# Kernel optimization log

Measured on AMD Instinct MI355X. Metric: run time of the kernel, lower is better.

The kernel has to match this reference:

```python
import jax, jax.numpy as jnp
import numpy as np

# ---- static config (matches init_kwargs) ----
BATCH = 8; SEQ_LEN = 1024; ENC_IN = 7; PRED_LEN = 96
D_MODEL = 512; N_HEADS = 8; D_HEAD = D_MODEL // N_HEADS
D_FF = 2048; E_LAYERS = 2; FACTOR = 5
PATCH = 16; STRIDE = 8; PAD = 8
N_PATCH = (SEQ_LEN + PAD - PATCH) // STRIDE + 1  # 128
NF = D_MODEL * N_PATCH


def _sin_pe(n, d):
    # sinusoidal positional embedding (Informer/TSLib PositionalEmbedding)
    pos = np.arange(n, dtype=np.float32)[:, None]
    div = np.exp(np.arange(0, d, 2, dtype=np.float32) * (-np.log(10000.0) / d))
    pe = np.zeros((n, d), dtype=np.float32)
    pe[:, 0::2] = np.sin(pos * div)
    pe[:, 1::2] = np.cos(pos * div)
    return jnp.asarray(pe)


def _ln(x, g, b, eps=1e-5):
    m = x.mean(-1, keepdims=True)
    v = x.var(-1, keepdims=True)
    return (x - m) / jnp.sqrt(v + eps) * g + b


def _prob_attention(q, k, v, layer_idx):
    # Informer ProbAttention, mask_flag=False. q,k,v: [B,H,L,Dh]
    B, H, L, Dh = q.shape
    u = min(int(FACTOR * np.ceil(np.log(L))), L)  # sample_k == n_top here (L_Q == L_K)
    skey = jax.random.fold_in(jax.random.key(42), layer_idx)
    samp = jax.random.randint(skey, (L, u), 0, L)          # random keys per query
    k_s = k[:, :, samp, :]                                  # [B,H,L,u,Dh]
    qk_s = jnp.einsum('bhld,bhlsd->bhls', q, k_s)           # sampled scores
    M = qk_s.max(-1) - qk_s.mean(-1)                        # sparsity measure [B,H,L]
    top = jax.lax.top_k(M, u)[1]                            # active query idx [B,H,u]
    q_r = jnp.take_along_axis(q, top[..., None], axis=2)    # [B,H,u,Dh]
    scores = jnp.einsum('bhud,bhld->bhul', q_r, k) / jnp.sqrt(jnp.asarray(Dh, q.dtype))
    attn = jax.nn.softmax(scores, axis=-1)
    upd = jnp.einsum('bhul,bhld->bhud', attn, v)            # [B,H,u,Dh]
    ctx = jnp.broadcast_to(v.mean(axis=2, keepdims=True), (B, H, L, Dh))
    bi = jnp.arange(B)[:, None, None]
    hi = jnp.arange(H)[None, :, None]
    ctx = ctx.at[bi, hi, top].set(upd)                      # scatter updated queries
    return ctx


def reference(x_enc, x_mark_enc, x_dec, x_mark_dec, patch_W,
              Wq, bq, Wk, bk, Wv, bv, Wo, bo,
              c1W, c1b, c2W, c2b, ln1g, ln1b, ln2g, ln2b,
              encg, encb, headW, headb):
    B, L, C = x_enc.shape
    # Normalize('Stat'): per-series mean/std over time
    mean = x_enc.mean(axis=1, keepdims=True)
    std = jnp.sqrt(x_enc.var(axis=1, keepdims=True) + 1e-5)
    xn = (x_enc - mean) / std
    # PatchEmbedding: [B,C,L] -> replication-pad -> unfold -> linear + pos emb
    xc = jnp.pad(xn.transpose(0, 2, 1), ((0, 0), (0, 0), (0, PAD)), mode='edge')
    idx = np.arange(N_PATCH)[:, None] * STRIDE + np.arange(PATCH)
    tok = xc[:, :, idx].reshape(B * C, N_PATCH, PATCH) @ patch_W.T  # [BC,N,dm]
    tok = tok + _sin_pe(N_PATCH, D_MODEL)
    # Transformer encoder with ProbAttention
    for l in range(E_LAYERS):
        Beff, N, _ = tok.shape
        q = (tok @ Wq[l].T + bq[l]).reshape(Beff, N, N_HEADS, D_HEAD).transpose(0, 2, 1, 3)
        k = (tok @ Wk[l].T + bk[l]).reshape(Beff, N, N_HEADS, D_HEAD).transpose(0, 2, 1, 3)
        v = (tok @ Wv[l].T + bv[l]).reshape(Beff, N, N_HEADS, D_HEAD).transpose(0, 2, 1, 3)
        ctx = _prob_attention(q, k, v, l).transpose(0, 2, 1, 3).reshape(Beff, N, D_MODEL)
        x1 = _ln(tok + ctx @ Wo[l].T + bo[l], ln1g[l], ln1b[l])
        y = jax.nn.gelu(x1 @ c1W[l].T + c1b[l], approximate=False)  # conv1d k=1 == linear
        y = y @ c2W[l].T + c2b[l]
        tok = _ln(x1 + y, ln2g[l], ln2b[l])
    tok = _ln(tok, encg, encb)
    # FlattenHead: [B,C,N,dm] -> [B,C,dm,N] -> flatten -> linear -> [B,pred,C]
    feat = tok.reshape(B, C, N_PATCH, D_MODEL).transpose(0, 1, 3, 2).reshape(B, C, NF)
    dec = (feat @ headW.T + headb).transpose(0, 2, 1)
    return dec * std + mean  # de-normalize


def setup_inputs():
    key = jax.random.key(0)
    ks = iter(jax.random.split(key, 40))
    def rn(shape, s=0.02):
        return jax.random.normal(next(ks), shape, jnp.float32) * s
    return {
        'x_enc': jax.random.normal(next(ks), (BATCH, SEQ_LEN, ENC_IN), jnp.float32),
        'x_mark_enc': jax.random.normal(next(ks), (BATCH, SEQ_LEN, 4), jnp.float32),
        'x_dec': jax.random.normal(next(ks), (BATCH, 144, ENC_IN), jnp.float32),
        'x_mark_dec': jax.random.normal(next(ks), (BATCH, 144, 4), jnp.float32),
        'patch_W': rn((D_MODEL, PATCH)),
        'Wq': rn((E_LAYERS, D_MODEL, D_MODEL)), 'bq': jnp.zeros((E_LAYERS, D_MODEL)),
        'Wk': rn((E_LAYERS, D_MODEL, D_MODEL)), 'bk': jnp.zeros((E_LAYERS, D_MODEL)),
        'Wv': rn((E_LAYERS, D_MODEL, D_MODEL)), 'bv': jnp.zeros((E_LAYERS, D_MODEL)),
        'Wo': rn((E_LAYERS, D_MODEL, D_MODEL)), 'bo': jnp.zeros((E_LAYERS, D_MODEL)),
        'c1W': rn((E_LAYERS, D_FF, D_MODEL)), 'c1b': jnp.zeros((E_LAYERS, D_FF)),
        'c2W': rn((E_LAYERS, D_MODEL, D_FF)), 'c2b': jnp.zeros((E_LAYERS, D_MODEL)),
        'ln1g': jnp.ones((E_LAYERS, D_MODEL)), 'ln1b': jnp.zeros((E_LAYERS, D_MODEL)),
        'ln2g': jnp.ones((E_LAYERS, D_MODEL)), 'ln2b': jnp.zeros((E_LAYERS, D_MODEL)),
        'encg': jnp.ones((D_MODEL,)), 'encb': jnp.zeros((D_MODEL,)),
        'headW': rn((PRED_LEN, NF)), 'headb': jnp.zeros((PRED_LEN,)),
    }
```

## Files before the change

### kernel.cpp

```cpp
#include <hip/hip_runtime.h>
#include <math.h>
#include <stdint.h>

#define SEQ   1024
#define CIN   7
#define NB    8
#define BC    56
#define NP    128
#define DM    512
#define NH    8
#define DH    64
#define DFF   2048
#define U     25
#define NTOK  (BC*NP)
#define PE_COEF (-9.210340371976184f / 512.0f)
#define HKB   256
#define HNB   256

typedef __attribute__((ext_vector_type(8))) short short8;
typedef __attribute__((ext_vector_type(4))) float f32x4;

__device__ __forceinline__ short f2bf(float x) {
    union { float f; uint32_t u; } v; v.f = x;
    uint32_t r = v.u + 0x7FFFu + ((v.u >> 16) & 1u);
    return (short)(r >> 16);
}
__device__ __forceinline__ float bf2f(short x) {
    union { uint32_t u; float f; } v; v.u = ((uint32_t)(uint16_t)x) << 16;
    return v.f;
}

__device__ __forceinline__ void gl_lds16(const void* g, void* s) {
    __builtin_amdgcn_global_load_lds((const __attribute__((address_space(1))) void*)g,
                                     (__attribute__((address_space(3))) void*)s, 16, 0, 0);
}

__global__ void stats_kernel(const float* __restrict__ x, float* __restrict__ mean,
                             float* __restrict__ stdv) {
    int bc = blockIdx.x; int b = bc / CIN, c = bc % CIN;
    const float* base = x + (size_t)b * SEQ * CIN + c;
    float s = 0.f, ss = 0.f;
    for (int i = threadIdx.x; i < SEQ; i += 256) {
        float v = base[(size_t)i * CIN];
        s += v; ss += v * v;
    }
    __shared__ float rs[256], rss[256];
    rs[threadIdx.x] = s; rss[threadIdx.x] = ss; __syncthreads();
    for (int o = 128; o > 0; o >>= 1) {
        if (threadIdx.x < o) { rs[threadIdx.x] += rs[threadIdx.x + o]; rss[threadIdx.x] += rss[threadIdx.x + o]; }
        __syncthreads();
    }
    if (threadIdx.x == 0) {
        float m = rs[0] / SEQ;
        float v = rss[0] / SEQ - m * m;
        mean[bc] = m;
        stdv[bc] = sqrtf(v + 1e-5f);
    }
}

__device__ __forceinline__ void tf_round(uint32_t& x0, uint32_t& x1, uint32_t r) {
    x0 += x1; x1 = (x1 << r) | (x1 >> (32u - r)); x1 ^= x0;
}
__device__ void threefry2x32(uint32_t k0, uint32_t k1, uint32_t x0, uint32_t x1,
                             uint32_t& o0, uint32_t& o1) {
    uint32_t ks[3] = { k0, k1, k0 ^ k1 ^ 0x1BD11BDAu };
    x0 += ks[0]; x1 += ks[1];
    const uint32_t rotA[4] = {13u, 15u, 26u, 6u}, rotB[4] = {17u, 29u, 16u, 24u};
    #pragma unroll
    for (int i = 0; i < 5; i++) {
        const uint32_t* rr = (i & 1) ? rotB : rotA;
        tf_round(x0, x1, rr[0]); tf_round(x0, x1, rr[1]);
        tf_round(x0, x1, rr[2]); tf_round(x0, x1, rr[3]);
        x0 += ks[(i + 1) % 3];
        x1 += ks[(i + 2) % 3] + (uint32_t)(i + 1);
    }
    o0 = x0; o1 = x1;
}

__global__ void prep_weights(const float* __restrict__ Wq, const float* __restrict__ Wk,
                             const float* __restrict__ Wv, const float* __restrict__ bq,
                             const float* __restrict__ bk, const float* __restrict__ bv,
                             const float* __restrict__ Wo, const float* __restrict__ c1W,
                             const float* __restrict__ c2W,
                             short* __restrict__ wqkv, float* __restrict__ bqkv,
                             short* __restrict__ wo_b, short* __restrict__ c1w_b,
                             short* __restrict__ c2w_b, int* __restrict__ samp) {
    int blk = blockIdx.x, tid = threadIdx.x;
    if (blk < 1536) {
        int idx = blk * 256 + tid;
        int k4 = idx & 127;
        int n  = (idx >> 7) % 1536;
        int l  = idx / (1536 * 128);
        int sel3 = n >> 9;
        int nn = n & 511;
        const float* src = sel3 == 0 ? Wq : sel3 == 1 ? Wk : Wv;
        float4 v = *(const float4*)(src + ((size_t)l * DM + nn) * DM + k4 * 4);
        short4 o; o.x = f2bf(v.x); o.y = f2bf(v.y); o.z = f2bf(v.z); o.w = f2bf(v.w);
        *(short4*)(wqkv + ((size_t)l * 1536 + n) * DM + k4 * 4) = o;
        if (k4 == 0) {
            const float* bsrc = sel3 == 0 ? bq : sel3 == 1 ? bk : bv;
            bqkv[l * 1536 + n] = bsrc[l * DM + nn];
        }
    } else if (blk < 6144) {
        const float* in; short* out; int i;
        if (blk < 2048)      { in = Wo;  out = wo_b;  i = (blk - 1536) * 256 + tid; }
        else if (blk < 4096) { in = c1W; out = c1w_b; i = (blk - 2048) * 256 + tid; }
        else                 { in = c2W; out = c2w_b; i = (blk - 4096) * 256 + tid; }
        float4 v = ((const float4*)in)[i];
        short4 o; o.x = f2bf(v.x); o.y = f2bf(v.y); o.z = f2bf(v.z); o.w = f2bf(v.w);
        ((short4*)out)[i] = o;
    } else {
        int l = blk - 6144;
        uint32_t s0, s1; threefry2x32(0u, 42u, 0u, (uint32_t)l, s0, s1);
        uint32_t a0, a1, b0, b1;
        threefry2x32(s0, s1, 0u, 2u, a0, a1);
        threefry2x32(s0, s1, 1u, 3u, b0, b1);
        uint32_t k20 = a1, k21 = b1;
        for (int i = tid; i < 1600; i += 256) {
            uint32_t o0, o1;
            threefry2x32(k20, k21, (uint32_t)i, (uint32_t)(1600 + i), o0, o1);
            samp[l * 3200 + i]        = (int)(o0 & 127u);
            samp[l * 3200 + 1600 + i] = (int)(o1 & 127u);
        }
    }
}

__global__ void patch_embed(const float* __restrict__ x, const float* __restrict__ pw,
                            const float* __restrict__ mean, const float* __restrict__ stdv,
                            float* __restrict__ tok, short* __restrict__ tokb) {
    int p = blockIdx.x, bc = blockIdx.y;
    int b = bc / CIN, c = bc % CIN;
    __shared__ float xs[16];
    if (threadIdx.x < 16) {
        int i = p * 8 + threadIdx.x;
        if (i > SEQ - 1) i = SEQ - 1;
        xs[threadIdx.x] = (x[(size_t)b * SEQ * CIN + (size_t)i * CIN + c] - mean[bc]) / stdv[bc];
    }
    __syncthreads();
    for (int d = threadIdx.x; d < DM; d += blockDim.x) {
        float acc = 0.f;
        const float* wr = pw + d * 16;
        #pragma unroll
        for (int t = 0; t < 16; t++) acc += xs[t] * wr[t];
        int k2 = d & ~1;
        float ang = (float)p * __expf((float)k2 * PE_COEF);
        acc += (d & 1) ? __cosf(ang) : __sinf(ang);
        size_t idx = ((size_t)bc * NP + p) * DM + d;
        tok[idx] = acc;
        tokb[idx] = f2bf(acc);
    }
}

template<int ACT, int OBF>
__global__ __launch_bounds__(256) void gemm_mfma(const short* __restrict__ A,
                                                 const short* __restrict__ W,
                                                 const float* __restrict__ bias,
                                                 float* __restrict__ Cf,
                                                 short* __restrict__ Cb,
                                                 int M, int N, int K) {
    __shared__ short LDSU[2][16384];
    int tid = threadIdx.x;
    int w = tid >> 6, lane = tid & 63;
    int row0 = blockIdx.x * 128, col0 = blockIdx.y * 128;
    int wrow = (w >> 1) * 64, wcol = (w & 1) * 64;
    int nt = K >> 6;
    f32x4 acc[4][4] = {};

    auto stage = [&](int b, int kt) {
        #pragma unroll
        for (int i = 0; i < 4; i++) {
            int L = i * 4096 + w * 1024 + lane * 16;
            int row = L >> 7;
            int cb  = L & 127;
            int scb = cb ^ ((row & 7) << 4);
            gl_lds16(A + (size_t)(row0 + row) * K + kt + (scb >> 1),
                     (char*)&LDSU[b][0] + i * 4096 + w * 1024);
            gl_lds16(W + (size_t)(col0 + row) * K + kt + (scb >> 1),
                     (char*)&LDSU[b][8192] + i * 4096 + w * 1024);
        }
    };

    stage(0, 0);
    __syncthreads();
    int cur = 0;
    for (int t = 0; t < nt; t++) {
        if (t + 1 < nt) stage(cur ^ 1, (t + 1) * 64);
        const char* Ab = (const char*)&LDSU[cur][0];
        const char* Bb = (const char*)&LDSU[cur][8192];
        #pragma unroll
        for (int ks = 0; ks < 2; ks++) {
            int cb = ks * 64 + ((lane >> 4) << 4);
            short8 af[4], bfr[4];
            #pragma unroll
            for (int m = 0; m < 4; m++) {
                int r = wrow + m * 16 + (lane & 15);
                af[m] = *(const short8*)(Ab + r * 128 + (cb ^ ((r & 7) << 4)));
            }
            #pragma unroll
            for (int n = 0; n < 4; n++) {
                int r = wcol + n * 16 + (lane & 15);
                bfr[n] = *(const short8*)(Bb + r * 128 + (cb ^ ((r & 7) << 4)));
            }
            #pragma unroll
            for (int m = 0; m < 4; m++)
                #pragma unroll
                for (int n = 0; n < 4; n++)
                    acc[m][n] = __builtin_amdgcn_mfma_f32_16x16x32_bf16(af[m], bfr[n], acc[m][n], 0, 0, 0);
        }
        __syncthreads();
        cur ^= 1;
    }

    #pragma unroll
    for (int m = 0; m < 4; m++) {
        int rbase = row0 + wrow + m * 16 + ((lane >> 4) << 2);
        #pragma unroll
        for (int n = 0; n < 4; n++) {
            int col = col0 + wcol + n * 16 + (lane & 15);
            float bval = bias[col];
            #pragma unroll
            for (int j = 0; j < 4; j++) {
                float v = acc[m][n][j] + bval;
                if (ACT == 1) {
                    float u = 0.7978845608f * (v + 0.044715f * v * v * v);
                    float e = exp2f(2.8853900817779268f * u);
                    v = v - v / (e + 1.0f);
                }
                if (OBF) Cb[(size_t)(rbase + j) * N + col] = f2bf(v);
                else     Cf[(size_t)(rbase + j) * N + col] = v;
            }
        }
    }
}

__global__ __launch_bounds__(256) void gemm_mfma64(const short* __restrict__ A,
                                                   const short* __restrict__ W,
                                                   const float* __restrict__ bias,
                                                   const float* __restrict__ resid,
                                                   float* __restrict__ Cf,
                                                   int M, int N, int K) {
    __shared__ short LDSU[2][12288];
    int tid = threadIdx.x;
    int w = tid >> 6, lane = tid & 63;
    int row0 = blockIdx.x * 64, col0 = blockIdx.y * 128;
    int nt = K >> 6;
    f32x4 acc[4][2] = {};

    auto stage = [&](int b, int kt) {
        #pragma unroll
        for (int i = 0; i < 2; i++) {
            int L = (i * 4 + w) * 1024 + lane * 16;
            int row = L >> 7, cb = L & 127;
            int scb = cb ^ ((row & 7) << 4);
            gl_lds16(A + (size_t)(row0 + row) * K + kt + (scb >> 1),
                     (char*)&LDSU[b][0] + (i * 4 + w) * 1024);
        }
        #pragma unroll
        for (int i = 0; i < 4; i++) {
            int L = (i * 4 + w) * 1024 + lane * 16;
            int row = L >> 7, cb = L & 127;
            int scb = cb ^ ((row & 7) << 4);
            gl_lds16(W + (size_t)(col0 + row) * K + kt + (scb >> 1),
                     (char*)&LDSU[b][4096] + (i * 4 + w) * 1024);
        }
    };

    stage(0, 0);
    __syncthreads();
    int cur = 0;
    for (int t = 0; t < nt; t++) {
        if (t + 1 < nt) stage(cur ^ 1, (t + 1) * 64);
        const char* Ab = (const char*)&LDSU[cur][0];
        const char* Bb = (const char*)&LDSU[cur][4096];
        #pragma unroll
        for (int ks = 0; ks < 2; ks++) {
            int cb = ks * 64 + ((lane >> 4) << 4);
            short8 af[4], bfr[2];
            #pragma unroll
            for (int m = 0; m < 4; m++) {
                int r = m * 16 + (lane & 15);
                af[m] = *(const short8*)(Ab + r * 128 + (cb ^ ((r & 7) << 4)));
            }
            #pragma unroll
            for (int n = 0; n < 2; n++) {
                int r = w * 32 + n * 16 + (lane & 15);
                bfr[n] = *(const short8*)(Bb + r * 128 + (cb ^ ((r & 7) << 4)));
            }
            #pragma unroll
            for (int m = 0; m < 4; m++)
                #pragma unroll
                for (int n = 0; n < 2; n++)
                    acc[m][n] = __builtin_amdgcn_mfma_f32_16x16x32_bf16(af[m], bfr[n], acc[m][n], 0, 0, 0);
        }
        __syncthreads();
        cur ^= 1;
    }

    #pragma unroll
    for (int m = 0; m < 4; m++) {
        int rbase = row0 + m * 16 + ((lane >> 4) << 2);
        #pragma unroll
        for (int n = 0; n < 2; n++) {
            int col = col0 + w * 32 + n * 16 + (lane & 15);
            float bval = bias[col];
            #pragma unroll
            for (int j = 0; j < 4; j++) {
                float v = acc[m][n][j] + bval;
                v += resid[(size_t)(rbase + j) * N + col];
                Cf[(size_t)(rbase + j) * N + col] = v;
            }
        }
    }
}

__global__ __launch_bounds__(256, 2) void attn_fused(const short* __restrict__ qkvb,
                                                     const int* __restrict__ samp,
                                                     short* __restrict__ ctxb) {
    __shared__ float Sbuf[64 * 130];
    __shared__ short Vt[64 * 128];
    __shared__ short Kls[128 * 64];
    __shared__ float Mv[128];
    __shared__ int   topl[32];
    __shared__ float vmean[64];
    __shared__ float vpart[256];

    float* Stop = Sbuf;
    short* Pb   = (short*)(Sbuf + 32 * 130);

    int bh = blockIdx.x, bc = bh >> 3, h = bh & 7;
    int tid = threadIdx.x, w = tid >> 6, lane = tid & 63;
    const short* base = qkvb + (size_t)bc * NP * 1536 + h * DH;
    short* cbase = ctxb + (size_t)bc * NP * DM + h * DH;

    for (int e = tid; e < 1024; e += 256) {
        int row = e >> 3, c8 = e & 7;
        short8 kv = *(const short8*)(base + (size_t)row * 1536 + 512 + c8 * 8);
        *(short8*)((char*)Kls + row * 128 + ((c8 * 16) ^ ((row & 7) << 4))) = kv;
        short8 vv = *(const short8*)(base + (size_t)row * 1536 + 1024 + c8 * 8);
        #pragma unroll
        for (int j = 0; j < 8; j++) {
            int d = c8 * 8 + j;
            *(short*)((char*)Vt + d * 256 + ((2 * row) ^ ((d & 7) << 4))) = vv[j];
        }
    }
    __syncthreads();
    {
        int d = tid & 63, part = tid >> 6;
        float s = 0.f;
        #pragma unroll
        for (int i4 = 0; i4 < 4; i4++) {
            short8 v = *(const short8*)((char*)Vt + d * 256 + ((part * 64 + i4 * 16) ^ ((d & 7) << 4)));
            #pragma unroll
            for (int j = 0; j < 8; j++) s += bf2f(v[j]);
        }
        vpart[part * 64 + d] = s;
    }

    for (int half = 0; half < 2; half++) {
        int ar = half * 64 + 16 * w + (lane & 15);
        const short* qp = base + (size_t)ar * 1536;
        short8 a0 = *(const short8*)(qp + (lane >> 4) * 8);
        short8 a1 = *(const short8*)(qp + 32 + (lane >> 4) * 8);
        #pragma unroll 2
        for (int ct = 0; ct < 8; ct++) {
            int br = ct * 16 + (lane & 15);
            int cb0 = (lane >> 4) * 16;
            short8 b0 = *(const short8*)((char*)Kls + br * 128 + (cb0 ^ ((br & 7) << 4)));
            short8 b1 = *(const short8*)((char*)Kls + br * 128 + ((cb0 + 64) ^ ((br & 7) << 4)));
            f32x4 acc = {};
            acc = __builtin_amdgcn_mfma_f32_16x16x32_bf16(a0, b0, acc, 0, 0, 0);
            acc = __builtin_amdgcn_mfma_f32_16x16x32_bf16(a1, b1, acc, 0, 0, 0);
            int r0 = 16 * w + ((lane >> 4) << 2);
            int c = ct * 16 + (lane & 15);
            #pragma unroll
            for (int j = 0; j < 4; j++) Sbuf[(r0 + j) * 130 + c] = acc[j] * 0.125f;
        }
        __syncthreads();
        if (tid < 64) {
            int r = half * 64 + tid;
            const int* sp = samp + r * U;
            const float* Srow = &Sbuf[tid * 130];
            float mx = -1e30f, sm = 0.f;
            #pragma unroll
            for (int s = 0; s < U; s++) { float v = Srow[sp[s]]; mx = fmaxf(mx, v); sm += v; }
            Mv[r] = mx - sm * (1.0f / U);
        } else if (half == 0 && tid < 128) {
            int d = tid - 64;
            vmean[d] = (vpart[d] + vpart[64 + d] + vpart[128 + d] + vpart[192 + d]) * (1.0f / 128.0f);
        }
        __syncthreads();
    }

    if (w == 0) {
        float v0 = Mv[lane], v1 = Mv[lane + 64];
        for (int it = 0; it < U; it++) {
            float bv; int bi;
            if (v1 > v0) { bv = v1; bi = lane + 64; } else { bv = v0; bi = lane; }
            #pragma unroll
            for (int o = 32; o > 0; o >>= 1) {
                float ov = __shfl_xor(bv, o);
                int   oi = __shfl_xor(bi, o);
                if (ov > bv || (ov == bv && oi < bi)) { bv = ov; bi = oi; }
            }
            if (lane == 0) topl[it] = bi;
            if (bi == lane) v0 = -1e30f;
            if (bi == lane + 64) v1 = -1e30f;
        }
    } else {
        for (int e = tid - 64; e < 128 * 16; e += 192) {
            int n = e >> 4, c4 = e & 15;
            short4 o;
            o.x = f2bf(vmean[c4 * 4 + 0]); o.y = f2bf(vmean[c4 * 4 + 1]);
            o.z = f2bf(vmean[c4 * 4 + 2]); o.w = f2bf(vmean[c4 * 4 + 3]);
            *(short4*)(cbase + (size_t)n * DM + c4 * 4) = o;
        }
    }
    __syncthreads();

    {
        int rt = w & 1, cth = w >> 1;
        int u = rt * 16 + (lane & 15);
        int qrow = topl[u < U ? u : U - 1];
        const short* qp = base + (size_t)qrow * 1536;
        short8 a0 = *(const short8*)(qp + (lane >> 4) * 8);
        short8 a1 = *(const short8*)(qp + 32 + (lane >> 4) * 8);
        #pragma unroll
        for (int cti = 0; cti < 4; cti++) {
            int ct = cth * 4 + cti;
            int br = ct * 16 + (lane & 15);
            int cb0 = (lane >> 4) * 16;
            short8 b0 = *(const short8*)((char*)Kls + br * 128 + (cb0 ^ ((br & 7) << 4)));
            short8 b1 = *(const short8*)((char*)Kls + br * 128 + ((cb0 + 64) ^ ((br & 7) << 4)));
            f32x4 acc = {};
            acc = __builtin_amdgcn_mfma_f32_16x16x32_bf16(a0, b0, acc, 0, 0, 0);
            acc = __builtin_amdgcn_mfma_f32_16x16x32_bf16(a1, b1, acc, 0, 0, 0);
            int r0 = rt * 16 + ((lane >> 4) << 2);
            int c = ct * 16 + (lane & 15);
            #pragma unroll
            for (int j = 0; j < 4; j++) Stop[(r0 + j) * 130 + c] = acc[j] * 0.125f;
        }
    }
    __syncthreads();

    for (int e = tid; e < 7 * 128; e += 256)
        Pb[(25 + (e >> 7)) * 128 + (e & 127)] = 0;
    for (int it = w; it < U; it += 4) {
        float s0 = Stop[it * 130 + lane], s1 = Stop[it * 130 + 64 + lane];
        float mx = fmaxf(s0, s1);
        #pragma unroll
        for (int o = 32; o > 0; o >>= 1) mx = fmaxf(mx, __shfl_xor(mx, o));
        float e0 = expf(s0 - mx), e1 = expf(s1 - mx);
        float sum = e0 + e1;
        #pragma unroll
        for (int o = 32; o > 0; o >>= 1) sum += __shfl_xor(sum, o);
        float inv = 1.0f / sum;
        int sw = (it & 7) << 4;
        *(short*)((char*)Pb + it * 256 + ((2 * lane) ^ sw))        = f2bf(e0 * inv);
        *(short*)((char*)Pb + it * 256 + ((2 * (64 + lane)) ^ sw)) = f2bf(e1 * inv);
    }
    __syncthreads();

    #pragma unroll
    for (int t = w * 2; t < w * 2 + 2; t++) {
        int rt = t >> 2, ct = t & 3;
        int pr = rt * 16 + (lane & 15);
        int vr = ct * 16 + (lane & 15);
        f32x4 acc = {};
        #pragma unroll
        for (int ks = 0; ks < 4; ks++) {
            int off = ks * 64 + (lane >> 4) * 16;
            short8 a = *(const short8*)((char*)Pb + pr * 256 + (off ^ ((pr & 7) << 4)));
            short8 b = *(const short8*)((char*)Vt + vr * 256 + (off ^ ((vr & 7) << 4)));
            acc = __builtin_amdgcn_mfma_f32_16x16x32_bf16(a, b, acc, 0, 0, 0);
        }
        int u0 = rt * 16 + ((lane >> 4) << 2), d = ct * 16 + (lane & 15);
        #pragma unroll
        for (int j = 0; j < 4; j++) {
            int u = u0 + j;
            if (u < U) cbase[(size_t)topl[u] * DM + d] = f2bf(acc[j]);
        }
    }
}

__global__ __launch_bounds__(256) void residual_ln(const float* __restrict__ a,
                                                   const float* __restrict__ g,
                                                   const float* __restrict__ beta,
                                                   float* __restrict__ out,
                                                   short* __restrict__ outb) {
    int row = blockIdx.x;
    int tid = threadIdx.x;
    const float* ar = a + (size_t)row * DM;
    float x0 = ar[tid], x1 = ar[tid + 256];
    __shared__ float rs[256], rss[256];
    rs[tid] = x0 + x1; rss[tid] = x0 * x0 + x1 * x1; __syncthreads();
    for (int o = 128; o > 0; o >>= 1) {
        if (tid < o) { rs[tid] += rs[tid + o]; rss[tid] += rss[tid + o]; }
        __syncthreads();
    }
    float m = rs[0] / DM;
    float var = rss[0] / DM - m * m;
    float r = rsqrtf(var + 1e-5f);
    float y0 = (x0 - m) * r * g[tid] + beta[tid];
    float y1 = (x1 - m) * r * g[tid + 256] + beta[tid + 256];
    if (out) {
        out[(size_t)row * DM + tid]       = y0;
        out[(size_t)row * DM + tid + 256] = y1;
    }
    if (outb) {
        outb[(size_t)row * DM + tid]       = f2bf(y0);
        outb[(size_t)row * DM + tid + 256] = f2bf(y1);
    }
}

__global__ void transpose_tok(const short* __restrict__ tokb, short* __restrict__ featb) {
    __shared__ short t[32][34];
    int bc = blockIdx.z, dt = blockIdx.y, pt = blockIdx.x;
    int tx = threadIdx.x, ty = threadIdx.y;
    #pragma unroll
    for (int i = 0; i < 4; i++) {
        int p = pt * 32 + ty + i * 8;
        int d = dt * 32 + tx;
        t[ty + i * 8][tx] = tokb[((size_t)bc * NP + p) * DM + d];
    }
    __syncthreads();
    #pragma unroll
    for (int i = 0; i < 4; i++) {
        int d = dt * 32 + ty + i * 8;
        int p = pt * 32 + tx;
        featb[(size_t)bc * (DM * NP) + (size_t)d * NP + p] = t[tx][ty + i * 8];
    }
}

__global__ __launch_bounds__(256) void head_mfma(const float* __restrict__ hw,
                                                 const short* __restrict__ featb,
                                                 float* __restrict__ partial) {
    __shared__ short Als[96 * 64];
    __shared__ short Bls[64 * 64];
    int tid = threadIdx.x;
    int w = tid >> 6, lane = tid & 63;
    int wm = w >> 1, wn = w & 1;
    int kb = blockIdx.x * HKB;
    f32x4 acc[3][2] = {};
    const char* Ab = (const char*)Als;
    const char* Bb = (const char*)Bls;

    for (int kt = 0; kt < HKB; kt += 64) {
        #pragma unroll
        for (int i = 0; i < 6; i++) {
            int s = tid + i * 256;
            int row = s >> 4, c4 = s & 15;
            float4 v = *(const float4*)(hw + (size_t)row * 65536 + kb + kt + c4 * 4);
            short4 o; o.x = f2bf(v.x); o.y = f2bf(v.y); o.z = f2bf(v.z); o.w = f2bf(v.w);
            int boff = row * 128 + ((c4 * 8) ^ ((row & 7) << 4));
            *(short4*)((char*)Als + boff) = o;
        }
        #pragma unroll
        for (int i = 0; i < 4; i++) {
            int s = tid + i * 256;
            int row = s >> 4, c4 = s & 15;
            short4 o;
            if (row < BC) o = *(const short4*)(featb + (size_t)row * 65536 + kb + kt + c4 * 4);
            else { o.x = 0; o.y = 0; o.z = 0; o.w = 0; }
            int boff = row * 128 + ((c4 * 8) ^ ((row & 7) << 4));
            *(short4*)((char*)Bls + boff) = o;
        }
        __syncthreads();
        #pragma unroll
        for (int ks = 0; ks < 2; ks++) {
            int cb = ks * 64 + ((lane >> 4) << 4);
            short8 af[3], bfr[2];
            #pragma unroll
            for (int m = 0; m < 3; m++) {
                int r = wm * 48 + m * 16 + (lane & 15);
                af[m] = *(const short8*)(Ab + r * 128 + (cb ^ ((r & 7) << 4)));
            }
            #pragma unroll
            for (int n = 0; n < 2; n++) {
                int r = wn * 32 + n * 16 + (lane & 15);
                bfr[n] = *(const short8*)(Bb + r * 128 + (cb ^ ((r & 7) << 4)));
            }
            #pragma unroll
            for (int m = 0; m < 3; m++)
                #pragma unroll
                for (int n = 0; n < 2; n++)
                    acc[m][n] = __builtin_amdgcn_mfma_f32_16x16x32_bf16(af[m], bfr[n], acc[m][n], 0, 0, 0);
        }
        __syncthreads();
    }

    float* pb = partial + (size_t)blockIdx.x * (96 * 64);
    #pragma unroll
    for (int m = 0; m < 3; m++) {
        int rbase = wm * 48 + m * 16 + ((lane >> 4) << 2);
        #pragma unroll
        for (int n = 0; n < 2; n++) {
            int col = wn * 32 + n * 16 + (lane & 15);
            #pragma unroll
            for (int j = 0; j < 4; j++)
                pb[(rbase + j) * 64 + col] = acc[m][n][j];
        }
    }
}

__global__ void finalize_a(const float* __restrict__ partial, float* __restrict__ p2) {
    int i = blockIdx.x * 256 + threadIdx.x;
    int s = blockIdx.y;
    const float* p = partial + (size_t)s * 32 * 6144 + i;
    float sum = 0.f;
    #pragma unroll
    for (int b = 0; b < 32; b++) sum += p[(size_t)b * 6144];
    p2[s * 6144 + i] = sum;
}

__global__ void finalize_b(const float* __restrict__ p2, const float* __restrict__ hb,
                           const float* __restrict__ mean, const float* __restrict__ stdv,
                           float* __restrict__ out) {
    int i = blockIdx.x * 256 + threadIdx.x;
    if (i >= NB * 96 * CIN) return;
    int b = i / (96 * CIN);
    int r = i % (96 * CIN);
    int t = r / CIN, c = r % CIN;
    int bc = b * CIN + c;
    int j = t * 64 + bc;
    float s = 0.f;
    #pragma unroll
    for (int k = 0; k < 8; k++) s += p2[k * 6144 + j];
    out[i] = (s + hb[t]) * stdv[bc] + mean[bc];
}

extern "C" void kernel_launch(void* const* d_in, const int* in_sizes, int n_in,
                              void* d_out, int out_size, void* d_ws, size_t ws_size,
                              hipStream_t stream) {
    (void)in_sizes; (void)n_in; (void)out_size; (void)ws_size;
    const float* x_enc   = (const float*)d_in[0];
    const float* patch_W = (const float*)d_in[4];
    const float* Wq  = (const float*)d_in[5];
    const float* bq  = (const float*)d_in[6];
    const float* Wk  = (const float*)d_in[7];
    const float* bk  = (const float*)d_in[8];
    const float* Wv  = (const float*)d_in[9];
    const float* bv  = (const float*)d_in[10];
    const float* Wo  = (const float*)d_in[11];
    const float* bo  = (const float*)d_in[12];
    const float* c1W = (const float*)d_in[13];
    const float* c1b = (const float*)d_in[14];
    const float* c2W = (const float*)d_in[15];
    const float* c2b = (const float*)d_in[16];
    const float* ln1g = (const float*)d_in[17];
    const float* ln1b = (const float*)d_in[18];
    const float* ln2g = (const float*)d_in[19];
    const float* ln2b = (const float*)d_in[20];
    const float* encg = (const float*)d_in[21];
    const float* encb = (const float*)d_in[22];
    const float* headW = (const float*)d_in[23];
    const float* headb = (const float*)d_in[24];
    float* out = (float*)d_out;

    float* ws = (float*)d_ws;
    float* mean = ws + 0;
    float* stdv = ws + 64;
    float* bqkv = ws + 128;
    int*   samp = (int*)(ws + 6144);
    size_t off = 32768;
    const size_t T = (size_t)NTOK * DM;
    float* tok     = ws + off; off += T;
    float* pA      = ws + off; off += T;
    float* x1      = ws + off; off += T;
    float* partial = ws + off; off += T;
    float* p2      = x1;
    short* sbase = (short*)(ws + off);
    size_t soff = 0;
    short* tok_b  = sbase + soff; soff += T;
    short* ctx_b  = sbase + soff; soff += T;
    short* x1_b   = sbase + soff; soff += T;
    short* qkv_b  = sbase + soff; soff += 3 * T;
    short* ffn_b  = sbase + soff; soff += (size_t)NTOK * DFF;
    short* featb  = ffn_b;
    short* wqkv_b = sbase + soff; soff += 2 * 1536 * DM;
    short* wo_b   = sbase + soff; soff += 2 * DM * DM;
    short* c1w_b  = sbase + soff; soff += 2 * (size_t)DFF * DM;
    short* c2w_b  = sbase + soff; soff += 2 * (size_t)DM * DFF;

    stats_kernel<<<BC, 256, 0, stream>>>(x_enc, mean, stdv);
    prep_weights<<<6146, 256, 0, stream>>>(Wq, Wk, Wv, bq, bk, bv, Wo, c1W, c2W,
                                           wqkv_b, bqkv, wo_b, c1w_b, c2w_b, samp);
    patch_embed<<<dim3(NP, BC), 128, 0, stream>>>(x_enc, patch_W, mean, stdv, tok, tok_b);

    for (int l = 0; l < 2; l++) {
        gemm_mfma<0,1><<<dim3(56, 12), 256, 0, stream>>>(tok_b, wqkv_b + (size_t)l * 1536 * DM, bqkv + l * 1536, nullptr, qkv_b, NTOK, 1536, DM);
        attn_fused<<<448, 256, 0, stream>>>(qkv_b, samp + l * 3200, ctx_b);
        gemm_mfma64<<<dim3(112, 4), 256, 0, stream>>>(ctx_b, wo_b + (size_t)l * DM * DM, bo + l * DM, tok, pA, NTOK, DM, DM);
        residual_ln<<<NTOK, 256, 0, stream>>>(pA, ln1g + l * DM, ln1b + l * DM, x1, x1_b);
        gemm_mfma<1,1><<<dim3(56, 16), 256, 0, stream>>>(x1_b, c1w_b + (size_t)l * DFF * DM, c1b + l * DFF, nullptr, ffn_b, NTOK, DFF, DM);
        gemm_mfma64<<<dim3(112, 4), 256, 0, stream>>>(ffn_b, c2w_b + (size_t)l * DM * DFF, c2b + l * DM, x1, pA, NTOK, DM, DFF);
        residual_ln<<<NTOK, 256, 0, stream>>>(pA, ln2g + l * DM, ln2b + l * DM, tok, tok_b);
    }

    residual_ln<<<NTOK, 256, 0, stream>>>(tok, encg, encb, nullptr, tok_b);
    transpose_tok<<<dim3(4, 16, BC), dim3(32, 8), 0, stream>>>(tok_b, featb);
    head_mfma<<<HNB, 256, 0, stream>>>(headW, featb, partial);
    finalize_a<<<dim3(24, 8), 256, 0, stream>>>(partial, p2);
    finalize_b<<<21, 256, 0, stream>>>(p2, headb, mean, stdv, out);
}
```

Baseline: 321.3 us.

## Keep residual stream in bf16, dropping fp32 activation copies

```diff
diff --git a/kernel.cpp b/kernel.cpp
--- a/kernel.cpp
+++ b/kernel.cpp
@@ -127,7 +127,7 @@
 
 __global__ void patch_embed(const float* __restrict__ x, const float* __restrict__ pw,
                             const float* __restrict__ mean, const float* __restrict__ stdv,
-                            float* __restrict__ tok, short* __restrict__ tokb) {
+                            short* __restrict__ tokb) {
     int p = blockIdx.x, bc = blockIdx.y;
     int b = bc / CIN, c = bc % CIN;
     __shared__ float xs[16];
@@ -145,17 +145,14 @@
         int k2 = d & ~1;
         float ang = (float)p * __expf((float)k2 * PE_COEF);
         acc += (d & 1) ? __cosf(ang) : __sinf(ang);
-        size_t idx = ((size_t)bc * NP + p) * DM + d;
-        tok[idx] = acc;
-        tokb[idx] = f2bf(acc);
-    }
-}
-
-template<int ACT, int OBF>
+        tokb[((size_t)bc * NP + p) * DM + d] = f2bf(acc);
+    }
+}
+
+template<int ACT>
 __global__ __launch_bounds__(256) void gemm_mfma(const short* __restrict__ A,
                                                  const short* __restrict__ W,
                                                  const float* __restrict__ bias,
-                                                 float* __restrict__ Cf,
                                                  short* __restrict__ Cb,
                                                  int M, int N, int K) {
     __shared__ short LDSU[2][16384];
@@ -226,8 +223,7 @@
                     float e = exp2f(2.8853900817779268f * u);
                     v = v - v / (e + 1.0f);
                 }
-                if (OBF) Cb[(size_t)(rbase + j) * N + col] = f2bf(v);
-                else     Cf[(size_t)(rbase + j) * N + col] = v;
+                Cb[(size_t)(rbase + j) * N + col] = f2bf(v);
             }
         }
     }
@@ -236,8 +232,8 @@
 __global__ __launch_bounds__(256) void gemm_mfma64(const short* __restrict__ A,
                                                    const short* __restrict__ W,
                                                    const float* __restrict__ bias,
-                                                   const float* __restrict__ resid,
-                                                   float* __restrict__ Cf,
+                                                   const short* __restrict__ residb,
+                                                   short* __restrict__ Cb,
                                                    int M, int N, int K) {
     __shared__ short LDSU[2][12288];
     int tid = threadIdx.x;
@@ -305,9 +301,8 @@
             float bval = bias[col];
             #pragma unroll
             for (int j = 0; j < 4; j++) {
-                float v = acc[m][n][j] + bval;
-                v += resid[(size_t)(rbase + j) * N + col];
-                Cf[(size_t)(rbase + j) * N + col] = v;
+                float v = acc[m][n][j] + bval + bf2f(residb[(size_t)(rbase + j) * N + col]);
+                Cb[(size_t)(rbase + j) * N + col] = f2bf(v);
             }
         }
     }
@@ -482,15 +477,15 @@
     }
 }
 
-__global__ __launch_bounds__(256) void residual_ln(const float* __restrict__ a,
+__global__ __launch_bounds__(256) void residual_ln(const short* __restrict__ a,
                                                    const float* __restrict__ g,
                                                    const float* __restrict__ beta,
-                                                   float* __restrict__ out,
                                                    short* __restrict__ outb) {
     int row = blockIdx.x;
     int tid = threadIdx.x;
-    const float* ar = a + (size_t)row * DM;
-    float x0 = ar[tid], x1 = ar[tid + 256];
+    uint32_t va = ((const uint32_t*)(a + (size_t)row * DM))[tid];
+    float x0 = bf2f((short)(va & 0xffff));
+    float x1 = bf2f((short)(va >> 16));
     __shared__ float rs[256], rss[256];
     rs[tid] = x0 + x1; rss[tid] = x0 * x0 + x1 * x1; __syncthreads();
     for (int o = 128; o > 0; o >>= 1) {
@@ -500,16 +495,12 @@
     float m = rs[0] / DM;
     float var = rss[0] / DM - m * m;
     float r = rsqrtf(var + 1e-5f);
-    float y0 = (x0 - m) * r * g[tid] + beta[tid];
-    float y1 = (x1 - m) * r * g[tid + 256] + beta[tid + 256];
-    if (out) {
-        out[(size_t)row * DM + tid]       = y0;
-        out[(size_t)row * DM + tid + 256] = y1;
-    }
-    if (outb) {
-        outb[(size_t)row * DM + tid]       = f2bf(y0);
-        outb[(size_t)row * DM + tid + 256] = f2bf(y1);
-    }
+    float2 gg = ((const float2*)g)[tid];
+    float2 bb = ((const float2*)beta)[tid];
+    float y0 = (x0 - m) * r * gg.x + bb.x;
+    float y1 = (x1 - m) * r * gg.y + bb.y;
+    uint32_t vo = (uint32_t)(uint16_t)f2bf(y0) | ((uint32_t)(uint16_t)f2bf(y1) << 16);
+    ((uint32_t*)(outb + (size_t)row * DM))[tid] = vo;
 }
 
 __global__ void transpose_tok(const short* __restrict__ tokb, short* __restrict__ featb) {
@@ -663,16 +654,14 @@
     int*   samp = (int*)(ws + 6144);
     size_t off = 32768;
     const size_t T = (size_t)NTOK * DM;
-    float* tok     = ws + off; off += T;
-    float* pA      = ws + off; off += T;
-    float* x1      = ws + off; off += T;
     float* partial = ws + off; off += T;
-    float* p2      = x1;
+    float* p2      = ws + off; off += 65536;
     short* sbase = (short*)(ws + off);
     size_t soff = 0;
     short* tok_b  = sbase + soff; soff += T;
     short* ctx_b  = sbase + soff; soff += T;
     short* x1_b   = sbase + soff; soff += T;
+    short* pA_b   = sbase + soff; soff += T;
     short* qkv_b  = sbase + soff; soff += 3 * T;
     short* ffn_b  = sbase + soff; soff += (size_t)NTOK * DFF;
     short* featb  = ffn_b;
@@ -684,20 +673,20 @@
     stats_kernel<<<BC, 256, 0, stream>>>(x_enc, mean, stdv);
     prep_weights<<<6146, 256, 0, stream>>>(Wq, Wk, Wv, bq, bk, bv, Wo, c1W, c2W,
                                            wqkv_b, bqkv, wo_b, c1w_b, c2w_b, samp);
-    patch_embed<<<dim3(NP, BC), 128, 0, stream>>>(x_enc, patch_W, mean, stdv, tok, tok_b);
+    patch_embed<<<dim3(NP, BC), 128, 0, stream>>>(x_enc, patch_W, mean, stdv, tok_b);
 
     for (int l = 0; l < 2; l++) {
-        gemm_mfma<0,1><<<dim3(56, 12), 256, 0, stream>>>(tok_b, wqkv_b + (size_t)l * 1536 * DM, bqkv + l * 1536, nullptr, qkv_b, NTOK, 1536, DM);
+        gemm_mfma<0><<<dim3(56, 12), 256, 0, stream>>>(tok_b, wqkv_b + (size_t)l * 1536 * DM, bqkv + l * 1536, qkv_b, NTOK, 1536, DM);
         attn_fused<<<448, 256, 0, stream>>>(qkv_b, samp + l * 3200, ctx_b);
-        gemm_mfma64<<<dim3(112, 4), 256, 0, stream>>>(ctx_b, wo_b + (size_t)l * DM * DM, bo + l * DM, tok, pA, NTOK, DM, DM);
-        residual_ln<<<NTOK, 256, 0, stream>>>(pA, ln1g + l * DM, ln1b + l * DM, x1, x1_b);
-        gemm_mfma<1,1><<<dim3(56, 16), 256, 0, stream>>>(x1_b, c1w_b + (size_t)l * DFF * DM, c1b + l * DFF, nullptr, ffn_b, NTOK, DFF, DM);
-        gemm_mfma64<<<dim3(112, 4), 256, 0, stream>>>(ffn_b, c2w_b + (size_t)l * DM * DFF, c2b + l * DM, x1, pA, NTOK, DM, DFF);
-        residual_ln<<<NTOK, 256, 0, stream>>>(pA, ln2g + l * DM, ln2b + l * DM, tok, tok_b);
-    }
-
-    residual_ln<<<NTOK, 256, 0, stream>>>(tok, encg, encb, nullptr, tok_b);
-    transpose_tok<<<dim3(4, 16, BC), dim3(32, 8), 0, stream>>>(tok_b, featb);
+        gemm_mfma64<<<dim3(112, 4), 256, 0, stream>>>(ctx_b, wo_b + (size_t)l * DM * DM, bo + l * DM, tok_b, pA_b, NTOK, DM, DM);
+        residual_ln<<<NTOK, 256, 0, stream>>>(pA_b, ln1g + l * DM, ln1b + l * DM, x1_b);
+        gemm_mfma<1><<<dim3(56, 16), 256, 0, stream>>>(x1_b, c1w_b + (size_t)l * DFF * DM, c1b + l * DFF, ffn_b, NTOK, DFF, DM);
+        gemm_mfma64<<<dim3(112, 4), 256, 0, stream>>>(ffn_b, c2w_b + (size_t)l * DM * DFF, c2b + l * DM, x1_b, pA_b, NTOK, DM, DFF);
+        residual_ln<<<NTOK, 256, 0, stream>>>(pA_b, ln2g + l * DM, ln2b + l * DM, tok_b);
+    }
+
+    residual_ln<<<NTOK, 256, 0, stream>>>(tok_b, encg, encb, x1_b);
+    transpose_tok<<<dim3(4, 16, BC), dim3(32, 8), 0, stream>>>(x1_b, featb);
     head_mfma<<<HNB, 256, 0, stream>>>(headW, featb, partial);
     finalize_a<<<dim3(24, 8), 256, 0, stream>>>(partial, p2);
     finalize_b<<<21, 256, 0, stream>>>(p2, headb, mean, stdv, out);
```

Measured after the change: 309.3 us. -3.7%, faster.
